# Kernel tuning notes

Hardware: AMD Instinct MI355X
Metric: run time of the kernel (lower is better)

The kernel has to match this reference:

```python
import jax, jax.numpy as jnp
import numpy as np

N = 50000
D = 512
H = 128
C = 32
E1 = 1600000
E2 = 3200000


def gcn_conv(x, W, b, src, dst, n_nodes):
    """PyG GCNConv: linear transform, add self-loops, symmetric norm, scatter-add, bias."""
    loop = jnp.arange(n_nodes, dtype=src.dtype)
    src = jnp.concatenate([src, loop])
    dst = jnp.concatenate([dst, loop])
    deg = jax.ops.segment_sum(jnp.ones_like(dst, dtype=x.dtype), dst, num_segments=n_nodes)
    dinv = jnp.where(deg > 0, jax.lax.rsqrt(deg), 0.0)
    norm = dinv[src] * dinv[dst]                    # [E+N]
    h = x @ W                                       # [N, out] dense GEMM first (PyG order)
    msg = h[src] * norm[:, None]                    # gather + scale, [E+N, out]
    out = jax.ops.segment_sum(msg, dst, num_segments=n_nodes)
    return out + b


def setup_inputs() -> dict:
    key = jax.random.key(0)
    ks = jax.random.split(key, 9)
    x = jax.random.normal(ks[0], (N, D), dtype=jnp.float32)
    edge_index = jax.random.randint(ks[1], (2, E1), 0, N, dtype=jnp.int64)
    sec_edge_index = jax.random.randint(ks[2], (2, E2), 0, N, dtype=jnp.int64)
    s1 = 1.0 / np.sqrt(D)
    s3 = 1.0 / np.sqrt(2 * H)
    W1 = jax.random.uniform(ks[3], (D, H), jnp.float32, -s1, s1)
    b1 = jnp.zeros((H,), jnp.float32)
    W2 = jax.random.uniform(ks[4], (D, H), jnp.float32, -s1, s1)
    b2 = jnp.zeros((H,), jnp.float32)
    W3 = jax.random.uniform(ks[5], (2 * H, C), jnp.float32, -s3, s3)
    b3 = jnp.zeros((C,), jnp.float32)
    return {"x": x, "edge_index": edge_index, "sec_edge_index": sec_edge_index,
            "W1": W1, "b1": b1, "W2": W2, "b2": b2, "W3": W3, "b3": b3}


def reference(x, edge_index, sec_edge_index, W1, b1, W2, b2, W3, b3):
    src1, dst1 = edge_index[0], edge_index[1]
    src2, dst2 = sec_edge_index[0], sec_edge_index[1]
    h1 = gcn_conv(x, W1, b1, src1, dst1, N)          # [N, H]
    h2 = gcn_conv(x, W2, b2, src2, dst2, N)          # [N, H]
    h = jax.nn.relu(jnp.concatenate([h1, h2], axis=-1))  # [N, 2H]
    # dropout is identity in eval mode
    out = gcn_conv(h, W3, b3, src1, dst1, N)         # [N, C]
    return jax.nn.log_softmax(out, axis=1)
```

## Files before the change

kernel.cpp:

```cpp
#include <hip/hip_runtime.h>

#define NNODES 50000
#define DIM 512
#define HID 128
#define NCLS 32
#define NBINS 196
#define CHUNK 8192
#define AGG_WAVES_G1 2048
#define AGG_WAVES_G2 4096
#define A3_WAVES 4096
#define HS_SCALE 64.0f
#define HS_ISCALE 0.015625f

typedef __attribute__((ext_vector_type(8))) short bf16x8;
typedef __attribute__((ext_vector_type(4))) float f32x4;
typedef __attribute__((ext_vector_type(2))) float f32x2;

__device__ __forceinline__ unsigned short f2bf(float f) {
    union { float f; unsigned int u; } a; a.f = f;
    unsigned int u = a.u;
    u += 0x7fff + ((u >> 16) & 1);
    return (unsigned short)(u >> 16);
}
__device__ __forceinline__ float bf2f(unsigned short h) {
    union { unsigned int u; float f; } a; a.u = ((unsigned int)h) << 16;
    return a.f;
}
__device__ __forceinline__ unsigned char f2fp8(float f) {
    int p = __builtin_amdgcn_cvt_pk_fp8_f32(f, 0.f, 0, false);
    return (unsigned char)(p & 0xff);
}
__device__ __forceinline__ void fp8add2(unsigned int u, f32x2& a01, f32x2& a23) {
    a01 += __builtin_amdgcn_cvt_pk_f32_fp8((int)u, false);
    a23 += __builtin_amdgcn_cvt_pk_f32_fp8((int)u, true);
}
__device__ __forceinline__ int lbound(const int* __restrict__ rp, int q) {
    int lo = 0, hi = NNODES;
    while (lo < hi) { int mid = (lo + hi) >> 1; if (rp[mid] >= q) hi = mid; else lo = mid + 1; }
    return lo;
}


__global__ __launch_bounds__(256)
void hist_kernel(const int* __restrict__ dst, int E, int nb, int* __restrict__ hist) {
    __shared__ int h[NBINS];
    int tid = threadIdx.x;
    for (int i = tid; i < NBINS; i += 256) h[i] = 0;
    __syncthreads();
    int e0 = blockIdx.x * CHUNK;
    int e1 = min(E, e0 + CHUNK);
    for (int e = e0 + tid; e < e1; e += 256)
        atomicAdd(&h[dst[e] >> 8], 1);
    __syncthreads();
    for (int i = tid; i < NBINS; i += 256)
        hist[(size_t)i * nb + blockIdx.x] = h[i];
}

__global__ __launch_bounds__(256)
void scan_row_kernel(int* __restrict__ data, int n, int* __restrict__ total) {
    int* row = data + (size_t)blockIdx.x * n;
    __shared__ int wsum[4];
    int tid = threadIdx.x, lane = tid & 63, wid = tid >> 6;
    int base = 0;
    for (int start = 0; start < n; start += 256) {
        int i = start + tid;
        int v = (i < n) ? row[i] : 0;
        int x = v;
        #pragma unroll
        for (int off = 1; off < 64; off <<= 1) {
            int t = __shfl_up(x, off);
            if (lane >= off) x += t;
        }
        if (lane == 63) wsum[wid] = x;
        __syncthreads();
        int woff = 0, tot = 0;
        #pragma unroll
        for (int w = 0; w < 4; ++w) { int s = wsum[w]; if (w < wid) woff += s; tot += s; }
        __syncthreads();
        if (i < n) row[i] = base + woff + x - v;
        base += tot;
    }
    if (tid == 0) total[blockIdx.x] = base;
}

__global__ __launch_bounds__(256)
void scatter_kernel(const int* __restrict__ src, const int* __restrict__ dst, int E, int nb,
                    const int* __restrict__ hist, const int* __restrict__ binStart,
                    unsigned int* __restrict__ binned) {
    __shared__ int cur[NBINS];
    int tid = threadIdx.x;
    for (int i = tid; i < NBINS; i += 256)
        cur[i] = hist[(size_t)i * nb + blockIdx.x] + binStart[i];
    __syncthreads();
    int e0 = blockIdx.x * CHUNK;
    int e1 = min(E, e0 + CHUNK);
    for (int e = e0 + tid; e < e1; e += 256) {
        int d = dst[e];
        int b = d >> 8;
        int p = atomicAdd(&cur[b], 1);
        binned[p] = ((unsigned int)(d & 255) << 16) | (unsigned int)src[e];
    }
}

__global__ __launch_bounds__(256)
void binfill_kernel(const unsigned int* __restrict__ binned, const int* __restrict__ binStart,
                    int* __restrict__ rowptr, float* __restrict__ dinv, int* __restrict__ col,
                    int totalE) {
    __shared__ int cnt[256], cur[256];
    __shared__ int wsum[4];
    int b = blockIdx.x;
    int tid = threadIdx.x, lane = tid & 63, wid = tid >> 6;
    int s = binStart[b], e = binStart[b + 1];
    cnt[tid] = 0;
    __syncthreads();
    for (int i = s + tid; i < e; i += 256)
        atomicAdd(&cnt[binned[i] >> 16], 1);
    __syncthreads();
    int v = cnt[tid];
    int x = v;
    #pragma unroll
    for (int off = 1; off < 64; off <<= 1) {
        int t = __shfl_up(x, off);
        if (lane >= off) x += t;
    }
    if (lane == 63) wsum[wid] = x;
    __syncthreads();
    int woff = 0;
    #pragma unroll
    for (int w = 0; w < 4; ++w) if (w < wid) woff += wsum[w];
    int ex = woff + x - v;
    cur[tid] = ex;
    __syncthreads();
    int node = b * 256 + tid;
    if (node < NNODES) {
        rowptr[node] = s + ex;
        dinv[node] = rsqrtf((float)v + 1.0f);
    }
    if (b == 0 && tid == 0) rowptr[NNODES] = totalE;
    for (int i = s + tid; i < e; i += 256) {
        unsigned int pk = binned[i];
        int ld = pk >> 16;
        int p = atomicAdd(&cur[ld], 1);
        col[s + p] = (int)(pk & 0xffff);
    }
}


__global__ __launch_bounds__(256)
void convW_kernel(const float* __restrict__ W1, const float* __restrict__ W2,
                  unsigned short* __restrict__ Wt2) {
    int k = blockIdx.x;
    int c = threadIdx.x;
    float v = (c < HID) ? W1[(size_t)k * HID + c] : W2[(size_t)k * HID + (c - HID)];
    int kt = k >> 5, kg = (k >> 3) & 3, kidx = k & 7;
    Wt2[(size_t)kt * 8192 + kg * 2048 + c * 8 + kidx] = f2bf(v);
}


__global__ __launch_bounds__(256)
void convW3_kernel(const float* __restrict__ W3, unsigned short* __restrict__ Wt3) {
    int idx = blockIdx.x * 256 + threadIdx.x;
    int k = idx >> 5, c = idx & 31;
    int kt = k >> 5, kg = (k >> 3) & 3, kidx = k & 7;
    Wt3[(kt * 4 + kg) * 256 + c * 8 + kidx] = f2bf(W3[(size_t)k * NCLS + c]);
}


__global__ __launch_bounds__(256)
void gemm12_mfma_kernel(const float* __restrict__ x, const unsigned short* __restrict__ Wt2,
                        const float* __restrict__ dinv1, const float* __restrict__ dinv2,
                        unsigned char* __restrict__ hs8) {
    __shared__ unsigned short Bs[2][8192];
    int tid = threadIdx.x;
    int wv = tid >> 6, l = tid & 63;
    int lr = l & 15, lg = l >> 4;
    int m0 = blockIdx.x * 64;
    int row = m0 + wv * 16 + lr;
    int rowc = min(row, NNODES - 1);
    const float* xrow = x + (size_t)rowc * DIM;

    f32x4 acc[16];
    #pragma unroll
    for (int n = 0; n < 16; ++n) acc[n] = (f32x4){0.f, 0.f, 0.f, 0.f};

    uint4 bn[4];
    float4 a0, a1, a0n, a1n;
    #pragma unroll
    for (int p = 0; p < 4; ++p)
        bn[p] = *(const uint4*)(Wt2 + p * 2048 + tid * 8);
    a0 = *(const float4*)(xrow + lg * 8);
    a1 = *(const float4*)(xrow + lg * 8 + 4);
    #pragma unroll
    for (int p = 0; p < 4; ++p)
        *(uint4*)(&Bs[0][p * 2048 + tid * 8]) = bn[p];
    __syncthreads();

    int cur = 0;
    for (int kt = 0; kt < 16; ++kt) {
        if (kt < 15) {
            #pragma unroll
            for (int p = 0; p < 4; ++p)
                bn[p] = *(const uint4*)(Wt2 + (size_t)(kt + 1) * 8192 + p * 2048 + tid * 8);
            a0n = *(const float4*)(xrow + (kt + 1) * 32 + lg * 8);
            a1n = *(const float4*)(xrow + (kt + 1) * 32 + lg * 8 + 4);
        }
        union { bf16x8 v; unsigned short u[8]; } af;
        af.u[0] = f2bf(a0.x); af.u[1] = f2bf(a0.y);
        af.u[2] = f2bf(a0.z); af.u[3] = f2bf(a0.w);
        af.u[4] = f2bf(a1.x); af.u[5] = f2bf(a1.y);
        af.u[6] = f2bf(a1.z); af.u[7] = f2bf(a1.w);
        #pragma unroll
        for (int nf = 0; nf < 16; ++nf) {
            bf16x8 bf = *(const bf16x8*)(&Bs[cur][lg * 2048 + (nf * 16 + lr) * 8]);
            acc[nf] = __builtin_amdgcn_mfma_f32_16x16x32_bf16(af.v, bf, acc[nf], 0, 0, 0);
        }
        if (kt < 15) {
            #pragma unroll
            for (int p = 0; p < 4; ++p)
                *(uint4*)(&Bs[cur ^ 1][p * 2048 + tid * 8]) = bn[p];
            __syncthreads();
            cur ^= 1;
            a0 = a0n; a1 = a1n;
        }
    }

    int row0 = m0 + wv * 16 + lg * 4;
    float d1[4], d2[4];
    #pragma unroll
    for (int j = 0; j < 4; ++j) {
        bool ok = (row0 + j) < NNODES;
        d1[j] = ok ? dinv1[row0 + j] * HS_SCALE : 0.f;
        d2[j] = ok ? dinv2[row0 + j] * HS_SCALE : 0.f;
    }
    #pragma unroll
    for (int nf = 0; nf < 16; ++nf) {
        int c = nf * 16 + lr;
        const float* d = (nf < 8) ? d1 : d2;
        #pragma unroll
        for (int j = 0; j < 4; ++j) {
            int r = row0 + j;
            if (r < NNODES)
                hs8[(size_t)r * 256 + c] = f2fp8(acc[nf][j] * d[j]);
        }
    }
}


__global__ __launch_bounds__(256)
void agg12_kernel(const unsigned char* __restrict__ hs8,
                  const int* __restrict__ rowptr1, const int* __restrict__ col1,
                  const int* __restrict__ rowptr2, const int* __restrict__ col2,
                  const float* __restrict__ dinv1, const float* __restrict__ dinv2,
                  const float* __restrict__ b1, const float* __restrict__ b2,
                  int E1, int E2, unsigned short* __restrict__ hcat) {
    int gw = blockIdx.x * 4 + (threadIdx.x >> 6);
    int lane = threadIdx.x & 63;
    int g, w, W; long long E;
    const int *rowptr, *col; const float *dinv, *bias;
    if (gw < AGG_WAVES_G1) {
        g = 0; w = gw; W = AGG_WAVES_G1; E = E1;
        rowptr = rowptr1; col = col1; dinv = dinv1; bias = b1;
    } else {
        g = 1; w = gw - AGG_WAVES_G1; W = AGG_WAVES_G2; E = E2;
        rowptr = rowptr2; col = col2; dinv = dinv2; bias = b2;
    }
    int q0 = (int)(E * w / W);
    int q1 = (int)(E * (w + 1) / W);
    int v0 = lbound(rowptr, q0);
    int v1 = (w == W - 1) ? NNODES : lbound(rowptr, q1);

    int quarter = lane >> 4;
    int lc = lane & 15;
    float bias8[8];
    #pragma unroll
    for (int j = 0; j < 8; ++j) bias8[j] = bias[lc * 8 + j];
    const unsigned char* hsg = hs8 + g * 128;

    for (int v = v0; v < v1; ++v) {
        int e0 = rowptr[v], e1 = rowptr[v + 1];
        f32x2 acc[4];
        #pragma unroll
        for (int i = 0; i < 4; ++i) acc[i] = (f32x2){0.f, 0.f};
        int e = e0;
        #pragma unroll 2
        for (; e + 8 <= e1; e += 8) {
            int sA = col[e + quarter];
            int sB = col[e + 4 + quarter];
            uint2 uA = *(const uint2*)(hsg + (size_t)sA * 256 + lc * 8);
            uint2 uB = *(const uint2*)(hsg + (size_t)sB * 256 + lc * 8);
            fp8add2(uA.x, acc[0], acc[1]); fp8add2(uA.y, acc[2], acc[3]);
            fp8add2(uB.x, acc[0], acc[1]); fp8add2(uB.y, acc[2], acc[3]);
        }
        if (e + 4 <= e1) {
            int sA = col[e + quarter];
            uint2 uA = *(const uint2*)(hsg + (size_t)sA * 256 + lc * 8);
            fp8add2(uA.x, acc[0], acc[1]); fp8add2(uA.y, acc[2], acc[3]);
            e += 4;
        }
        if (e < e1 && quarter < e1 - e) {
            int sA = col[e + quarter];
            uint2 uA = *(const uint2*)(hsg + (size_t)sA * 256 + lc * 8);
            fp8add2(uA.x, acc[0], acc[1]); fp8add2(uA.y, acc[2], acc[3]);
        }
        #pragma unroll
        for (int i = 0; i < 4; ++i) {
            #pragma unroll
            for (int off = 16; off <= 32; off <<= 1) {
                acc[i][0] += __shfl_xor(acc[i][0], off);
                acc[i][1] += __shfl_xor(acc[i][1], off);
            }
        }
        uint2 su = *(const uint2*)(hsg + (size_t)v * 256 + lc * 8);
        fp8add2(su.x, acc[0], acc[1]); fp8add2(su.y, acc[2], acc[3]);
        float sc = dinv[v] * HS_ISCALE;
        if (quarter == 0) {
            unsigned int res[4];
            #pragma unroll
            for (int p = 0; p < 4; ++p) {
                float r0 = fmaxf(acc[p][0] * sc + bias8[2 * p + 0], 0.f);
                float r1 = fmaxf(acc[p][1] * sc + bias8[2 * p + 1], 0.f);
                res[p] = (unsigned int)f2bf(r0) | ((unsigned int)f2bf(r1) << 16);
            }
            uint4 st = {res[0], res[1], res[2], res[3]};
            *(uint4*)(hcat + (size_t)v * 256 + g * 128 + lc * 8) = st;
        }
    }
}


__global__ __launch_bounds__(256)
void gemm3_mfma_kernel(const unsigned short* __restrict__ hcat,
                       const unsigned short* __restrict__ Wt3,
                       const float* __restrict__ dinv1, unsigned short* __restrict__ gs) {
    __shared__ unsigned short Ws[8192];
    int tid = threadIdx.x;
    #pragma unroll
    for (int p = 0; p < 4; ++p)
        *(uint4*)(&Ws[p * 2048 + tid * 8]) = *(const uint4*)(Wt3 + p * 2048 + tid * 8);
    __syncthreads();

    int wv = tid >> 6, l = tid & 63;
    int lr = l & 15, lg = l >> 4;
    int rbase = blockIdx.x * 256 + wv * 64;

    f32x4 acc[4][2];
    #pragma unroll
    for (int m = 0; m < 4; ++m)
        #pragma unroll
        for (int n = 0; n < 2; ++n)
            acc[m][n] = (f32x4){0.f, 0.f, 0.f, 0.f};

    #pragma unroll
    for (int kt = 0; kt < 8; ++kt) {
        #pragma unroll
        for (int m = 0; m < 4; ++m) {
            int rA = min(rbase + m * 16 + lr, NNODES - 1);
            bf16x8 af = *(const bf16x8*)(hcat + (size_t)rA * 256 + kt * 32 + lg * 8);
            #pragma unroll
            for (int n = 0; n < 2; ++n) {
                bf16x8 bf = *(const bf16x8*)(&Ws[(kt * 4 + lg) * 256 + (n * 16 + lr) * 8]);
                acc[m][n] = __builtin_amdgcn_mfma_f32_16x16x32_bf16(af, bf, acc[m][n], 0, 0, 0);
            }
        }
    }

    #pragma unroll
    for (int m = 0; m < 4; ++m) {
        int row0 = rbase + m * 16 + lg * 4;
        float d[4];
        #pragma unroll
        for (int j = 0; j < 4; ++j)
            d[j] = (row0 + j < NNODES) ? dinv1[row0 + j] : 0.f;
        #pragma unroll
        for (int n = 0; n < 2; ++n) {
            int c = n * 16 + lr;
            #pragma unroll
            for (int j = 0; j < 4; ++j) {
                int r = row0 + j;
                if (r < NNODES)
                    gs[(size_t)r * 32 + c] = f2bf(acc[m][n][j] * d[j]);
            }
        }
    }
}


__global__ __launch_bounds__(256)
void agg3_kernel(const unsigned short* __restrict__ gs, const int* __restrict__ rowptr1,
                 const int* __restrict__ col1, const float* __restrict__ dinv1,
                 const float* __restrict__ b3, float* __restrict__ out, int E1) {
    int gw = blockIdx.x * 4 + (threadIdx.x >> 6);
    int lane = threadIdx.x & 63;
    long long E = E1;
    int q0 = (int)(E * gw / A3_WAVES);
    int q1 = (int)(E * (gw + 1) / A3_WAVES);
    int v0 = lbound(rowptr1, q0);
    int v1 = (gw == A3_WAVES - 1) ? NNODES : lbound(rowptr1, q1);

    int oct = lane >> 3;
    int lc = lane & 7;
    float4 b3v = *(const float4*)(b3 + lc * 4);

    for (int v = v0; v < v1; ++v) {
        int e0 = rowptr1[v], e1 = rowptr1[v + 1];
        float a0 = 0.f, a1 = 0.f, a2 = 0.f, a3 = 0.f;
        int e = e0;
        #pragma unroll 2
        for (; e + 8 <= e1; e += 8) {
            int srco = col1[e + oct];
            uint2 u = *(const uint2*)(gs + (size_t)srco * 32 + lc * 4);
            a0 += bf2f((unsigned short)(u.x & 0xffff));
            a1 += bf2f((unsigned short)(u.x >> 16));
            a2 += bf2f((unsigned short)(u.y & 0xffff));
            a3 += bf2f((unsigned short)(u.y >> 16));
        }
        if (e < e1) {
            int r = e1 - e;
            if (oct < r) {
                int srco = col1[e + oct];
                uint2 u = *(const uint2*)(gs + (size_t)srco * 32 + lc * 4);
                a0 += bf2f((unsigned short)(u.x & 0xffff));
                a1 += bf2f((unsigned short)(u.x >> 16));
                a2 += bf2f((unsigned short)(u.y & 0xffff));
                a3 += bf2f((unsigned short)(u.y >> 16));
            }
        }
        #pragma unroll
        for (int off = 32; off >= 8; off >>= 1) {
            a0 += __shfl_xor(a0, off); a1 += __shfl_xor(a1, off);
            a2 += __shfl_xor(a2, off); a3 += __shfl_xor(a3, off);
        }
        uint2 su = *(const uint2*)(gs + (size_t)v * 32 + lc * 4);
        a0 += bf2f((unsigned short)(su.x & 0xffff));
        a1 += bf2f((unsigned short)(su.x >> 16));
        a2 += bf2f((unsigned short)(su.y & 0xffff));
        a3 += bf2f((unsigned short)(su.y >> 16));
        float d = dinv1[v];
        float l0 = a0 * d + b3v.x, l1 = a1 * d + b3v.y;
        float l2 = a2 * d + b3v.z, l3 = a3 * d + b3v.w;
        float m = fmaxf(fmaxf(l0, l1), fmaxf(l2, l3));
        #pragma unroll
        for (int off = 1; off <= 4; off <<= 1) m = fmaxf(m, __shfl_xor(m, off));
        float s = expf(l0 - m) + expf(l1 - m) + expf(l2 - m) + expf(l3 - m);
        #pragma unroll
        for (int off = 1; off <= 4; off <<= 1) s += __shfl_xor(s, off);
        float lg = logf(s);
        if (oct == 0) {
            float4 o = make_float4(l0 - m - lg, l1 - m - lg, l2 - m - lg, l3 - m - lg);
            *(float4*)(out + (size_t)v * 32 + lc * 4) = o;
        }
    }
}

extern "C" void kernel_launch(void* const* d_in, const int* in_sizes, int n_in,
                              void* d_out, int out_size, void* d_ws, size_t ws_size,
                              hipStream_t stream) {
    const float* x  = (const float*)d_in[0];
    const int* ei1  = (const int*)d_in[1];
    const int* ei2  = (const int*)d_in[2];
    const float* W1 = (const float*)d_in[3];
    const float* b1 = (const float*)d_in[4];
    const float* W2 = (const float*)d_in[5];
    const float* b2 = (const float*)d_in[6];
    const float* W3 = (const float*)d_in[7];
    const float* b3 = (const float*)d_in[8];
    float* out = (float*)d_out;

    int E1 = in_sizes[1] / 2;
    int E2 = in_sizes[2] / 2;
    const int* src1 = ei1;       const int* dst1 = ei1 + E1;
    const int* src2 = ei2;       const int* dst2 = ei2 + E2;
    int nb1 = (E1 + CHUNK - 1) / CHUNK;
    int nb2 = (E2 + CHUNK - 1) / CHUNK;

    char* w = (char*)d_ws;
    auto alloc = [&](size_t bytes) -> char* {
        char* p = w; w += (bytes + 255) & ~(size_t)255; return p;
    };
    int* hist1   = (int*)alloc((size_t)NBINS * nb1 * 4);
    int* hist2   = (int*)alloc((size_t)NBINS * nb2 * 4);
    int* bs1     = (int*)alloc((size_t)(NBINS + 1) * 4);
    int* bs2     = (int*)alloc((size_t)(NBINS + 1) * 4);
    int* rowptr1 = (int*)alloc((size_t)(NNODES + 1) * 4);
    int* rowptr2 = (int*)alloc((size_t)(NNODES + 1) * 4);
    float* dinv1 = (float*)alloc((size_t)NNODES * 4);
    float* dinv2 = (float*)alloc((size_t)NNODES * 4);
    int* col1    = (int*)alloc((size_t)E1 * 4);
    int* col2    = (int*)alloc((size_t)E2 * 4);
    unsigned short* Wt2 = (unsigned short*)alloc((size_t)256 * DIM * 2);
    unsigned short* Wt3 = (unsigned short*)alloc((size_t)256 * NCLS * 2);
    unsigned char* hs8 = (unsigned char*)alloc((size_t)NNODES * 256);
    unsigned short* gs = (unsigned short*)alloc((size_t)NNODES * 32 * 2);
    unsigned short* hcat = (unsigned short*)alloc((size_t)NNODES * 256 * 2);
    unsigned int* binned1 = (unsigned int*)hcat;
    unsigned int* binned2 = binned1 + E1;

    hist_kernel<<<nb1, 256, 0, stream>>>(dst1, E1, nb1, hist1);
    hist_kernel<<<nb2, 256, 0, stream>>>(dst2, E2, nb2, hist2);
    scan_row_kernel<<<NBINS, 256, 0, stream>>>(hist1, nb1, bs1);
    scan_row_kernel<<<NBINS, 256, 0, stream>>>(hist2, nb2, bs2);
    scan_row_kernel<<<1, 256, 0, stream>>>(bs1, NBINS, bs1 + NBINS);
    scan_row_kernel<<<1, 256, 0, stream>>>(bs2, NBINS, bs2 + NBINS);
    scatter_kernel<<<nb1, 256, 0, stream>>>(src1, dst1, E1, nb1, hist1, bs1, binned1);
    scatter_kernel<<<nb2, 256, 0, stream>>>(src2, dst2, E2, nb2, hist2, bs2, binned2);
    binfill_kernel<<<NBINS, 256, 0, stream>>>(binned1, bs1, rowptr1, dinv1, col1, E1);
    binfill_kernel<<<NBINS, 256, 0, stream>>>(binned2, bs2, rowptr2, dinv2, col2, E2);

    convW_kernel<<<DIM, 256, 0, stream>>>(W1, W2, Wt2);
    convW3_kernel<<<32, 256, 0, stream>>>(W3, Wt3);
    gemm12_mfma_kernel<<<(NNODES + 63) / 64, 256, 0, stream>>>(x, Wt2, dinv1, dinv2, hs8);
    agg12_kernel<<<(AGG_WAVES_G1 + AGG_WAVES_G2) / 4, 256, 0, stream>>>(
        hs8, rowptr1, col1, rowptr2, col2, dinv1, dinv2, b1, b2, E1, E2, hcat);
    gemm3_mfma_kernel<<<(NNODES + 255) / 256, 256, 0, stream>>>(hcat, Wt3, dinv1, gs);
    agg3_kernel<<<A3_WAVES / 4, 256, 0, stream>>>(gs, rowptr1, col1, dinv1, b3, out, E1);
}
```

Measured before the change: 365.4 us.

## Merge graph-build kernels across both graphs and split per-bin fill into slices

```diff
diff --git a/kernel.cpp b/kernel.cpp
--- a/kernel.cpp
+++ b/kernel.cpp
@@ -5,10 +5,11 @@
 #define HID 128
 #define NCLS 32
 #define NBINS 196
-#define CHUNK 8192
-#define AGG_WAVES_G1 2048
-#define AGG_WAVES_G2 4096
-#define A3_WAVES 4096
+#define CHUNK 4096
+#define PB 4
+#define AGG_WAVES_G1 4096
+#define AGG_WAVES_G2 8192
+#define A3_WAVES 8192
 #define HS_SCALE 64.0f
 #define HS_ISCALE 0.015625f
 
@@ -39,26 +40,7 @@
     while (lo < hi) { int mid = (lo + hi) >> 1; if (rp[mid] >= q) hi = mid; else lo = mid + 1; }
     return lo;
 }
-
-
-__global__ __launch_bounds__(256)
-void hist_kernel(const int* __restrict__ dst, int E, int nb, int* __restrict__ hist) {
-    __shared__ int h[NBINS];
-    int tid = threadIdx.x;
-    for (int i = tid; i < NBINS; i += 256) h[i] = 0;
-    __syncthreads();
-    int e0 = blockIdx.x * CHUNK;
-    int e1 = min(E, e0 + CHUNK);
-    for (int e = e0 + tid; e < e1; e += 256)
-        atomicAdd(&h[dst[e] >> 8], 1);
-    __syncthreads();
-    for (int i = tid; i < NBINS; i += 256)
-        hist[(size_t)i * nb + blockIdx.x] = h[i];
-}
-
-__global__ __launch_bounds__(256)
-void scan_row_kernel(int* __restrict__ data, int n, int* __restrict__ total) {
-    int* row = data + (size_t)blockIdx.x * n;
+__device__ __forceinline__ void scan_inplace(int* __restrict__ row, int n, int* __restrict__ total) {
     __shared__ int wsum[4];
     int tid = threadIdx.x, lane = tid & 63, wid = tid >> 6;
     int base = 0;
@@ -80,43 +62,108 @@
         if (i < n) row[i] = base + woff + x - v;
         base += tot;
     }
-    if (tid == 0) total[blockIdx.x] = base;
-}
-
-__global__ __launch_bounds__(256)
-void scatter_kernel(const int* __restrict__ src, const int* __restrict__ dst, int E, int nb,
-                    const int* __restrict__ hist, const int* __restrict__ binStart,
-                    unsigned int* __restrict__ binned) {
+    if (tid == 0) *total = base;
+}
+
+
+__global__ __launch_bounds__(256)
+void hist2_kernel(const int* __restrict__ dst1, int E1, int nb1, int* __restrict__ hist1,
+                  const int* __restrict__ dst2, int E2, int nb2, int* __restrict__ hist2) {
+    __shared__ int h[NBINS];
+    int blk = blockIdx.x;
+    const int* dst; int E, nb, b; int* hist;
+    if (blk < nb1) { dst = dst1; E = E1; nb = nb1; b = blk; hist = hist1; }
+    else { dst = dst2; E = E2; nb = nb2; b = blk - nb1; hist = hist2; }
+    int tid = threadIdx.x;
+    for (int i = tid; i < NBINS; i += 256) h[i] = 0;
+    __syncthreads();
+    int e0 = b * CHUNK;
+    int e1 = min(E, e0 + CHUNK);
+    for (int e = e0 + tid; e < e1; e += 256)
+        atomicAdd(&h[dst[e] >> 8], 1);
+    __syncthreads();
+    for (int i = tid; i < NBINS; i += 256)
+        hist[(size_t)i * nb + b] = h[i];
+}
+
+__global__ __launch_bounds__(256)
+void scanrow2_kernel(int* __restrict__ hist1, int nb1, int* __restrict__ bs1,
+                     int* __restrict__ hist2, int nb2, int* __restrict__ bs2) {
+    int b = blockIdx.x;
+    if (b < NBINS) scan_inplace(hist1 + (size_t)b * nb1, nb1, bs1 + b);
+    else           scan_inplace(hist2 + (size_t)(b - NBINS) * nb2, nb2, bs2 + (b - NBINS));
+}
+
+__global__ __launch_bounds__(256)
+void scanbs_kernel(int* __restrict__ bs1, int* __restrict__ bs2) {
+    if (blockIdx.x == 0) scan_inplace(bs1, NBINS, bs1 + NBINS);
+    else                 scan_inplace(bs2, NBINS, bs2 + NBINS);
+}
+
+__global__ __launch_bounds__(256)
+void scatter2_kernel(const int* __restrict__ src1, const int* __restrict__ dst1, int E1, int nb1,
+                     const int* __restrict__ hist1, const int* __restrict__ bs1,
+                     unsigned int* __restrict__ binned1,
+                     const int* __restrict__ src2, const int* __restrict__ dst2, int E2, int nb2,
+                     const int* __restrict__ hist2, const int* __restrict__ bs2,
+                     unsigned int* __restrict__ binned2) {
     __shared__ int cur[NBINS];
+    int blk = blockIdx.x;
+    const int *src, *dst, *hist, *bs; int E, nb, b; unsigned int* binned;
+    if (blk < nb1) { src = src1; dst = dst1; E = E1; nb = nb1; b = blk; hist = hist1; bs = bs1; binned = binned1; }
+    else { src = src2; dst = dst2; E = E2; nb = nb2; b = blk - nb1; hist = hist2; bs = bs2; binned = binned2; }
     int tid = threadIdx.x;
     for (int i = tid; i < NBINS; i += 256)
-        cur[i] = hist[(size_t)i * nb + blockIdx.x] + binStart[i];
-    __syncthreads();
-    int e0 = blockIdx.x * CHUNK;
+        cur[i] = hist[(size_t)i * nb + b] + bs[i];
+    __syncthreads();
+    int e0 = b * CHUNK;
     int e1 = min(E, e0 + CHUNK);
     for (int e = e0 + tid; e < e1; e += 256) {
         int d = dst[e];
-        int b = d >> 8;
-        int p = atomicAdd(&cur[b], 1);
+        int bb = d >> 8;
+        int p = atomicAdd(&cur[bb], 1);
         binned[p] = ((unsigned int)(d & 255) << 16) | (unsigned int)src[e];
     }
 }
 
 __global__ __launch_bounds__(256)
-void binfill_kernel(const unsigned int* __restrict__ binned, const int* __restrict__ binStart,
-                    int* __restrict__ rowptr, float* __restrict__ dinv, int* __restrict__ col,
-                    int totalE) {
-    __shared__ int cnt[256], cur[256];
+void count2_kernel(const unsigned int* __restrict__ binned1, const int* __restrict__ bs1,
+                   int* __restrict__ cnt1,
+                   const unsigned int* __restrict__ binned2, const int* __restrict__ bs2,
+                   int* __restrict__ cnt2, int nblk1) {
+    __shared__ int h[256];
+    int blk = blockIdx.x;
+    const unsigned int* binned; const int* bs; int* cnt;
+    if (blk < nblk1) { binned = binned1; bs = bs1; cnt = cnt1; }
+    else { blk -= nblk1; binned = binned2; bs = bs2; cnt = cnt2; }
+    int bin = blk / PB, slice = blk % PB;
+    int s = bs[bin], len = bs[bin + 1] - s;
+    int i0 = s + (int)((long long)len * slice / PB);
+    int i1 = s + (int)((long long)len * (slice + 1) / PB);
+    int tid = threadIdx.x;
+    h[tid] = 0;
+    __syncthreads();
+    for (int i = i0 + tid; i < i1; i += 256)
+        atomicAdd(&h[binned[i] >> 16], 1);
+    __syncthreads();
+    int v = h[tid];
+    if (v) atomicAdd(&cnt[bin * 256 + tid], v);
+}
+
+__global__ __launch_bounds__(256)
+void binscan2_kernel(const int* __restrict__ cnt1, const int* __restrict__ bs1,
+                     int* __restrict__ rowptr1, float* __restrict__ dinv1,
+                     int* __restrict__ cur1, int E1,
+                     const int* __restrict__ cnt2, const int* __restrict__ bs2,
+                     int* __restrict__ rowptr2, float* __restrict__ dinv2,
+                     int* __restrict__ cur2, int E2) {
     __shared__ int wsum[4];
     int b = blockIdx.x;
+    const int *cnt, *bs; int* rowptr; float* dinv; int* cur; int E;
+    if (b < NBINS) { cnt = cnt1; bs = bs1; rowptr = rowptr1; dinv = dinv1; cur = cur1; E = E1; }
+    else { b -= NBINS; cnt = cnt2; bs = bs2; rowptr = rowptr2; dinv = dinv2; cur = cur2; E = E2; }
     int tid = threadIdx.x, lane = tid & 63, wid = tid >> 6;
-    int s = binStart[b], e = binStart[b + 1];
-    cnt[tid] = 0;
-    __syncthreads();
-    for (int i = s + tid; i < e; i += 256)
-        atomicAdd(&cnt[binned[i] >> 16], 1);
-    __syncthreads();
-    int v = cnt[tid];
+    int v = cnt[b * 256 + tid];
     int x = v;
     #pragma unroll
     for (int off = 1; off < 64; off <<= 1) {
@@ -128,20 +175,34 @@
     int woff = 0;
     #pragma unroll
     for (int w = 0; w < 4; ++w) if (w < wid) woff += wsum[w];
-    int ex = woff + x - v;
-    cur[tid] = ex;
-    __syncthreads();
+    int pos = bs[b] + woff + x - v;
     int node = b * 256 + tid;
+    cur[b * 256 + tid] = pos;
     if (node < NNODES) {
-        rowptr[node] = s + ex;
+        rowptr[node] = pos;
         dinv[node] = rsqrtf((float)v + 1.0f);
     }
-    if (b == 0 && tid == 0) rowptr[NNODES] = totalE;
-    for (int i = s + tid; i < e; i += 256) {
+    if (b == NBINS - 1 && tid == 0) rowptr[NNODES] = E;
+}
+
+__global__ __launch_bounds__(256)
+void place2_kernel(const unsigned int* __restrict__ binned1, const int* __restrict__ bs1,
+                   int* __restrict__ cur1, int* __restrict__ col1,
+                   const unsigned int* __restrict__ binned2, const int* __restrict__ bs2,
+                   int* __restrict__ cur2, int* __restrict__ col2, int nblk1) {
+    int blk = blockIdx.x;
+    const unsigned int* binned; const int* bs; int *cur, *col;
+    if (blk < nblk1) { binned = binned1; bs = bs1; cur = cur1; col = col1; }
+    else { blk -= nblk1; binned = binned2; bs = bs2; cur = cur2; col = col2; }
+    int bin = blk / PB, slice = blk % PB;
+    int s = bs[bin], len = bs[bin + 1] - s;
+    int i0 = s + (int)((long long)len * slice / PB);
+    int i1 = s + (int)((long long)len * (slice + 1) / PB);
+    for (int i = i0 + threadIdx.x; i < i1; i += 256) {
         unsigned int pk = binned[i];
         int ld = pk >> 16;
-        int p = atomicAdd(&cur[ld], 1);
-        col[s + p] = (int)(pk & 0xffff);
+        int p = atomicAdd(&cur[bin * 256 + ld], 1);
+        col[p] = (int)(pk & 0xffff);
     }
 }
 
@@ -485,6 +546,10 @@
     int* rowptr2 = (int*)alloc((size_t)(NNODES + 1) * 4);
     float* dinv1 = (float*)alloc((size_t)NNODES * 4);
     float* dinv2 = (float*)alloc((size_t)NNODES * 4);
+    int* cnt1    = (int*)alloc((size_t)NBINS * 256 * 4);
+    int* cnt2    = (int*)alloc((size_t)NBINS * 256 * 4);
+    int* cur1    = (int*)alloc((size_t)NBINS * 256 * 4);
+    int* cur2    = (int*)alloc((size_t)NBINS * 256 * 4);
     int* col1    = (int*)alloc((size_t)E1 * 4);
     int* col2    = (int*)alloc((size_t)E2 * 4);
     unsigned short* Wt2 = (unsigned short*)alloc((size_t)256 * DIM * 2);
@@ -495,16 +560,20 @@
     unsigned int* binned1 = (unsigned int*)hcat;
     unsigned int* binned2 = binned1 + E1;
 
-    hist_kernel<<<nb1, 256, 0, stream>>>(dst1, E1, nb1, hist1);
-    hist_kernel<<<nb2, 256, 0, stream>>>(dst2, E2, nb2, hist2);
-    scan_row_kernel<<<NBINS, 256, 0, stream>>>(hist1, nb1, bs1);
-    scan_row_kernel<<<NBINS, 256, 0, stream>>>(hist2, nb2, bs2);
-    scan_row_kernel<<<1, 256, 0, stream>>>(bs1, NBINS, bs1 + NBINS);
-    scan_row_kernel<<<1, 256, 0, stream>>>(bs2, NBINS, bs2 + NBINS);
-    scatter_kernel<<<nb1, 256, 0, stream>>>(src1, dst1, E1, nb1, hist1, bs1, binned1);
-    scatter_kernel<<<nb2, 256, 0, stream>>>(src2, dst2, E2, nb2, hist2, bs2, binned2);
-    binfill_kernel<<<NBINS, 256, 0, stream>>>(binned1, bs1, rowptr1, dinv1, col1, E1);
-    binfill_kernel<<<NBINS, 256, 0, stream>>>(binned2, bs2, rowptr2, dinv2, col2, E2);
+    hipMemsetAsync(cnt1, 0, (size_t)NBINS * 256 * 4, stream);
+    hipMemsetAsync(cnt2, 0, (size_t)NBINS * 256 * 4, stream);
+
+    hist2_kernel<<<nb1 + nb2, 256, 0, stream>>>(dst1, E1, nb1, hist1, dst2, E2, nb2, hist2);
+    scanrow2_kernel<<<NBINS * 2, 256, 0, stream>>>(hist1, nb1, bs1, hist2, nb2, bs2);
+    scanbs_kernel<<<2, 256, 0, stream>>>(bs1, bs2);
+    scatter2_kernel<<<nb1 + nb2, 256, 0, stream>>>(src1, dst1, E1, nb1, hist1, bs1, binned1,
+                                                   src2, dst2, E2, nb2, hist2, bs2, binned2);
+    count2_kernel<<<NBINS * PB * 2, 256, 0, stream>>>(binned1, bs1, cnt1,
+                                                      binned2, bs2, cnt2, NBINS * PB);
+    binscan2_kernel<<<NBINS * 2, 256, 0, stream>>>(cnt1, bs1, rowptr1, dinv1, cur1, E1,
+                                                   cnt2, bs2, rowptr2, dinv2, cur2, E2);
+    place2_kernel<<<NBINS * PB * 2, 256, 0, stream>>>(binned1, bs1, cur1, col1,
+                                                      binned2, bs2, cur2, col2, NBINS * PB);
 
     convW_kernel<<<DIM, 256, 0, stream>>>(W1, W2, Wt2);
     convW3_kernel<<<32, 256, 0, stream>>>(W3, Wt3);
```

Result: slower. 391.8 us (+7.2%).

## Merge paired CSR-build launches and widen agg12 per-lane loads to 16 bytes

Applied to the files above, without the earlier changes.

```diff
diff --git a/kernel.cpp b/kernel.cpp
--- a/kernel.cpp
+++ b/kernel.cpp
@@ -39,26 +39,7 @@
     while (lo < hi) { int mid = (lo + hi) >> 1; if (rp[mid] >= q) hi = mid; else lo = mid + 1; }
     return lo;
 }
-
-
-__global__ __launch_bounds__(256)
-void hist_kernel(const int* __restrict__ dst, int E, int nb, int* __restrict__ hist) {
-    __shared__ int h[NBINS];
-    int tid = threadIdx.x;
-    for (int i = tid; i < NBINS; i += 256) h[i] = 0;
-    __syncthreads();
-    int e0 = blockIdx.x * CHUNK;
-    int e1 = min(E, e0 + CHUNK);
-    for (int e = e0 + tid; e < e1; e += 256)
-        atomicAdd(&h[dst[e] >> 8], 1);
-    __syncthreads();
-    for (int i = tid; i < NBINS; i += 256)
-        hist[(size_t)i * nb + blockIdx.x] = h[i];
-}
-
-__global__ __launch_bounds__(256)
-void scan_row_kernel(int* __restrict__ data, int n, int* __restrict__ total) {
-    int* row = data + (size_t)blockIdx.x * n;
+__device__ __forceinline__ void scan_inplace(int* __restrict__ row, int n, int* __restrict__ total) {
     __shared__ int wsum[4];
     int tid = threadIdx.x, lane = tid & 63, wid = tid >> 6;
     int base = 0;
@@ -80,37 +61,85 @@
         if (i < n) row[i] = base + woff + x - v;
         base += tot;
     }
-    if (tid == 0) total[blockIdx.x] = base;
-}
-
-__global__ __launch_bounds__(256)
-void scatter_kernel(const int* __restrict__ src, const int* __restrict__ dst, int E, int nb,
-                    const int* __restrict__ hist, const int* __restrict__ binStart,
-                    unsigned int* __restrict__ binned) {
+    if (tid == 0) *total = base;
+}
+
+
+__global__ __launch_bounds__(256)
+void hist2_kernel(const int* __restrict__ dst1, int E1, int nb1, int* __restrict__ hist1,
+                  const int* __restrict__ dst2, int E2, int nb2, int* __restrict__ hist2) {
+    __shared__ int h[NBINS];
+    int blk = blockIdx.x;
+    const int* dst; int E, nb, b; int* hist;
+    if (blk < nb1) { dst = dst1; E = E1; nb = nb1; b = blk; hist = hist1; }
+    else { dst = dst2; E = E2; nb = nb2; b = blk - nb1; hist = hist2; }
+    int tid = threadIdx.x;
+    for (int i = tid; i < NBINS; i += 256) h[i] = 0;
+    __syncthreads();
+    int e0 = b * CHUNK;
+    int e1 = min(E, e0 + CHUNK);
+    for (int e = e0 + tid; e < e1; e += 256)
+        atomicAdd(&h[dst[e] >> 8], 1);
+    __syncthreads();
+    for (int i = tid; i < NBINS; i += 256)
+        hist[(size_t)i * nb + b] = h[i];
+}
+
+__global__ __launch_bounds__(256)
+void scanrow2_kernel(int* __restrict__ hist1, int nb1, int* __restrict__ bs1,
+                     int* __restrict__ hist2, int nb2, int* __restrict__ bs2) {
+    int b = blockIdx.x;
+    if (b < NBINS) scan_inplace(hist1 + (size_t)b * nb1, nb1, bs1 + b);
+    else           scan_inplace(hist2 + (size_t)(b - NBINS) * nb2, nb2, bs2 + (b - NBINS));
+}
+
+__global__ __launch_bounds__(256)
+void scanbs_kernel(int* __restrict__ bs1, int* __restrict__ bs2) {
+    if (blockIdx.x == 0) scan_inplace(bs1, NBINS, bs1 + NBINS);
+    else                 scan_inplace(bs2, NBINS, bs2 + NBINS);
+}
+
+__global__ __launch_bounds__(256)
+void scatter2_kernel(const int* __restrict__ src1, const int* __restrict__ dst1, int E1, int nb1,
+                     const int* __restrict__ hist1, const int* __restrict__ bs1,
+                     unsigned int* __restrict__ binned1,
+                     const int* __restrict__ src2, const int* __restrict__ dst2, int E2, int nb2,
+                     const int* __restrict__ hist2, const int* __restrict__ bs2,
+                     unsigned int* __restrict__ binned2) {
     __shared__ int cur[NBINS];
+    int blk = blockIdx.x;
+    const int *src, *dst, *hist, *bs; int E, nb, b; unsigned int* binned;
+    if (blk < nb1) { src = src1; dst = dst1; E = E1; nb = nb1; b = blk; hist = hist1; bs = bs1; binned = binned1; }
+    else { src = src2; dst = dst2; E = E2; nb = nb2; b = blk - nb1; hist = hist2; bs = bs2; binned = binned2; }
     int tid = threadIdx.x;
     for (int i = tid; i < NBINS; i += 256)
-        cur[i] = hist[(size_t)i * nb + blockIdx.x] + binStart[i];
-    __syncthreads();
-    int e0 = blockIdx.x * CHUNK;
+        cur[i] = hist[(size_t)i * nb + b] + bs[i];
+    __syncthreads();
+    int e0 = b * CHUNK;
     int e1 = min(E, e0 + CHUNK);
     for (int e = e0 + tid; e < e1; e += 256) {
         int d = dst[e];
-        int b = d >> 8;
-        int p = atomicAdd(&cur[b], 1);
+        int bb = d >> 8;
+        int p = atomicAdd(&cur[bb], 1);
         binned[p] = ((unsigned int)(d & 255) << 16) | (unsigned int)src[e];
     }
 }
 
 __global__ __launch_bounds__(256)
-void binfill_kernel(const unsigned int* __restrict__ binned, const int* __restrict__ binStart,
-                    int* __restrict__ rowptr, float* __restrict__ dinv, int* __restrict__ col,
-                    int totalE) {
+void binfill2_kernel(const unsigned int* __restrict__ binned1, const int* __restrict__ bs1,
+                     int* __restrict__ rowptr1, float* __restrict__ dinv1,
+                     int* __restrict__ col1, int E1,
+                     const unsigned int* __restrict__ binned2, const int* __restrict__ bs2,
+                     int* __restrict__ rowptr2, float* __restrict__ dinv2,
+                     int* __restrict__ col2, int E2) {
     __shared__ int cnt[256], cur[256];
     __shared__ int wsum[4];
     int b = blockIdx.x;
+    const unsigned int* binned; const int* bs; int* rowptr; float* dinv; int* col; int totalE;
+    if (b < NBINS) { binned = binned1; bs = bs1; rowptr = rowptr1; dinv = dinv1; col = col1; totalE = E1; }
+    else { b -= NBINS; binned = binned2; bs = bs2; rowptr = rowptr2; dinv = dinv2; col = col2; totalE = E2; }
     int tid = threadIdx.x, lane = tid & 63, wid = tid >> 6;
-    int s = binStart[b], e = binStart[b + 1];
+    int s = bs[b], e = bs[b + 1];
     cnt[tid] = 0;
     __syncthreads();
     for (int i = s + tid; i < e; i += 256)
@@ -269,60 +298,67 @@
     int v0 = lbound(rowptr, q0);
     int v1 = (w == W - 1) ? NNODES : lbound(rowptr, q1);
 
-    int quarter = lane >> 4;
-    int lc = lane & 15;
-    float bias8[8];
-    #pragma unroll
-    for (int j = 0; j < 8; ++j) bias8[j] = bias[lc * 8 + j];
+    int oct = lane >> 3;
+    int lc = lane & 7;
+    float bias16[16];
+    #pragma unroll
+    for (int j = 0; j < 16; ++j) bias16[j] = bias[lc * 16 + j];
     const unsigned char* hsg = hs8 + g * 128;
 
     for (int v = v0; v < v1; ++v) {
         int e0 = rowptr[v], e1 = rowptr[v + 1];
-        f32x2 acc[4];
-        #pragma unroll
-        for (int i = 0; i < 4; ++i) acc[i] = (f32x2){0.f, 0.f};
+        f32x2 acc[8];
+        #pragma unroll
+        for (int i = 0; i < 8; ++i) acc[i] = (f32x2){0.f, 0.f};
         int e = e0;
-        #pragma unroll 2
-        for (; e + 8 <= e1; e += 8) {
-            int sA = col[e + quarter];
-            int sB = col[e + 4 + quarter];
-            uint2 uA = *(const uint2*)(hsg + (size_t)sA * 256 + lc * 8);
-            uint2 uB = *(const uint2*)(hsg + (size_t)sB * 256 + lc * 8);
+        for (; e + 16 <= e1; e += 16) {
+            int sA = col[e + oct];
+            int sB = col[e + 8 + oct];
+            uint4 uA = *(const uint4*)(hsg + (size_t)sA * 256 + lc * 16);
+            uint4 uB = *(const uint4*)(hsg + (size_t)sB * 256 + lc * 16);
             fp8add2(uA.x, acc[0], acc[1]); fp8add2(uA.y, acc[2], acc[3]);
+            fp8add2(uA.z, acc[4], acc[5]); fp8add2(uA.w, acc[6], acc[7]);
             fp8add2(uB.x, acc[0], acc[1]); fp8add2(uB.y, acc[2], acc[3]);
-        }
-        if (e + 4 <= e1) {
-            int sA = col[e + quarter];
-            uint2 uA = *(const uint2*)(hsg + (size_t)sA * 256 + lc * 8);
+            fp8add2(uB.z, acc[4], acc[5]); fp8add2(uB.w, acc[6], acc[7]);
+        }
+        if (e + 8 <= e1) {
+            int sA = col[e + oct];
+            uint4 uA = *(const uint4*)(hsg + (size_t)sA * 256 + lc * 16);
             fp8add2(uA.x, acc[0], acc[1]); fp8add2(uA.y, acc[2], acc[3]);
-            e += 4;
-        }
-        if (e < e1 && quarter < e1 - e) {
-            int sA = col[e + quarter];
-            uint2 uA = *(const uint2*)(hsg + (size_t)sA * 256 + lc * 8);
+            fp8add2(uA.z, acc[4], acc[5]); fp8add2(uA.w, acc[6], acc[7]);
+            e += 8;
+        }
+        if (e < e1 && oct < e1 - e) {
+            int sA = col[e + oct];
+            uint4 uA = *(const uint4*)(hsg + (size_t)sA * 256 + lc * 16);
             fp8add2(uA.x, acc[0], acc[1]); fp8add2(uA.y, acc[2], acc[3]);
-        }
-        #pragma unroll
-        for (int i = 0; i < 4; ++i) {
+            fp8add2(uA.z, acc[4], acc[5]); fp8add2(uA.w, acc[6], acc[7]);
+        }
+        #pragma unroll
+        for (int i = 0; i < 8; ++i) {
             #pragma unroll
-            for (int off = 16; off <= 32; off <<= 1) {
+            for (int off = 8; off <= 32; off <<= 1) {
                 acc[i][0] += __shfl_xor(acc[i][0], off);
                 acc[i][1] += __shfl_xor(acc[i][1], off);
             }
         }
-        uint2 su = *(const uint2*)(hsg + (size_t)v * 256 + lc * 8);
+        uint4 su = *(const uint4*)(hsg + (size_t)v * 256 + lc * 16);
         fp8add2(su.x, acc[0], acc[1]); fp8add2(su.y, acc[2], acc[3]);
+        fp8add2(su.z, acc[4], acc[5]); fp8add2(su.w, acc[6], acc[7]);
         float sc = dinv[v] * HS_ISCALE;
-        if (quarter == 0) {
-            unsigned int res[4];
+        if (oct == 0) {
+            unsigned int res[8];
             #pragma unroll
-            for (int p = 0; p < 4; ++p) {
-                float r0 = fmaxf(acc[p][0] * sc + bias8[2 * p + 0], 0.f);
-                float r1 = fmaxf(acc[p][1] * sc + bias8[2 * p + 1], 0.f);
+            for (int p = 0; p < 8; ++p) {
+                float r0 = fmaxf(acc[p][0] * sc + bias16[2 * p + 0], 0.f);
+                float r1 = fmaxf(acc[p][1] * sc + bias16[2 * p + 1], 0.f);
                 res[p] = (unsigned int)f2bf(r0) | ((unsigned int)f2bf(r1) << 16);
             }
-            uint4 st = {res[0], res[1], res[2], res[3]};
-            *(uint4*)(hcat + (size_t)v * 256 + g * 128 + lc * 8) = st;
+            unsigned short* dst = hcat + (size_t)v * 256 + g * 128 + lc * 16;
+            uint4 st0 = {res[0], res[1], res[2], res[3]};
+            uint4 st1 = {res[4], res[5], res[6], res[7]};
+            *(uint4*)(dst) = st0;
+            *(uint4*)(dst + 8) = st1;
         }
     }
 }
@@ -495,16 +531,13 @@
     unsigned int* binned1 = (unsigned int*)hcat;
     unsigned int* binned2 = binned1 + E1;
 
-    hist_kernel<<<nb1, 256, 0, stream>>>(dst1, E1, nb1, hist1);
-    hist_kernel<<<nb2, 256, 0, stream>>>(dst2, E2, nb2, hist2);
-    scan_row_kernel<<<NBINS, 256, 0, stream>>>(hist1, nb1, bs1);
-    scan_row_kernel<<<NBINS, 256, 0, stream>>>(hist2, nb2, bs2);
-    scan_row_kernel<<<1, 256, 0, stream>>>(bs1, NBINS, bs1 + NBINS);
-    scan_row_kernel<<<1, 256, 0, stream>>>(bs2, NBINS, bs2 + NBINS);
-    scatter_kernel<<<nb1, 256, 0, stream>>>(src1, dst1, E1, nb1, hist1, bs1, binned1);
-    scatter_kernel<<<nb2, 256, 0, stream>>>(src2, dst2, E2, nb2, hist2, bs2, binned2);
-    binfill_kernel<<<NBINS, 256, 0, stream>>>(binned1, bs1, rowptr1, dinv1, col1, E1);
-    binfill_kernel<<<NBINS, 256, 0, stream>>>(binned2, bs2, rowptr2, dinv2, col2, E2);
+    hist2_kernel<<<nb1 + nb2, 256, 0, stream>>>(dst1, E1, nb1, hist1, dst2, E2, nb2, hist2);
+    scanrow2_kernel<<<NBINS * 2, 256, 0, stream>>>(hist1, nb1, bs1, hist2, nb2, bs2);
+    scanbs_kernel<<<2, 256, 0, stream>>>(bs1, bs2);
+    scatter2_kernel<<<nb1 + nb2, 256, 0, stream>>>(src1, dst1, E1, nb1, hist1, bs1, binned1,
+                                                   src2, dst2, E2, nb2, hist2, bs2, binned2);
+    binfill2_kernel<<<NBINS * 2, 256, 0, stream>>>(binned1, bs1, rowptr1, dinv1, col1, E1,
+                                                   binned2, bs2, rowptr2, dinv2, col2, E2);
 
     convW_kernel<<<DIM, 256, 0, stream>>>(W1, W2, Wt2);
     convW3_kernel<<<32, 256, 0, stream>>>(W3, Wt3);
```

Measured after the change: 369.6 us. About the same (+1.2%).
